# Optimization experiments

Hardware: AMD Instinct MI355X
Metric: run time of the kernel (lower is better)

Reference implementation:

```python
import jax, jax.numpy as jnp
import numpy as np

B, T, L = 512, 512, 128  # batch, seq_len, tag-vocab size (incl. START=126, STOP=127)


def setup_inputs() -> dict:
    key = jax.random.key(0)
    k1, k2, k3 = jax.random.split(key, 3)
    # scale emissions so exp(gold path score) stays finite in fp32
    feats = jax.random.normal(k1, (B, T, L), dtype=jnp.float32) * 0.05
    # xavier_normal on [L, L] -> std = sqrt(2/(L+L)) = 1/sqrt(L)
    transfer = jax.random.normal(k2, (L, L), dtype=jnp.float32) * (1.0 / np.sqrt(L))
    target = jax.random.randint(k3, (B, T), 0, L - 2, dtype=jnp.int32)
    return {"feats": feats, "transfer": transfer, "target": target,
            "start": L - 2, "stop": L - 1}


def _crf_loss(feats, transfer, target, start, stop):
    # feats: [B, T, L] emissions; transfer: [L, L]; target: [B, T] gold tags
    Bb, Tt, Ll = feats.shape

    # ---- forward algorithm (log-sum-exp DP over tags) ----
    # scores[1] = feats[1] + transfer[start, :]
    prev0 = feats[:, 1] + transfer[start][None, :]  # [B, L]

    def step(prev, f_t):
        # original: scores[t, y] = LSE_x( scores[t-1, x] + feats[t, x] + transfer[x, y] )
        v = prev + f_t                                        # [B, L] over prev-tag x
        new = jax.nn.logsumexp(v[:, :, None] + transfer[None, :, :], axis=1)  # [B, L]
        return new, None

    step = jax.checkpoint(step)  # keep scan residuals to just the carries
    feats_rest = jnp.swapaxes(feats[:, 2:], 0, 1)  # [T-2, B, L]
    prev, _ = jax.lax.scan(step, prev0, feats_rest)
    sentence_score = jax.nn.logsumexp(prev + transfer[:, stop][None, :], axis=1)  # [B]

    # ---- gold path score ----
    emit0 = feats[:, 0, start]  # hh[0, start]
    emit = jnp.take_along_axis(feats[:, 1:], target[:, 1:, None], axis=2)[..., 0].sum(axis=1)
    pre = jnp.concatenate(
        [jnp.full((Bb, 1), start, dtype=target.dtype), target[:, 1:Tt - 1]], axis=1)  # [B, T-1]
    # original reads transfer[pre, tgt].data[0] -> detached constant
    trans = jax.lax.stop_gradient(transfer[pre, target[:, 1:]]).sum(axis=1)
    gold_score = jnp.exp(emit0 + emit + trans)  # original returns torch.exp(score)

    return sentence_score - gold_score  # per-sentence loss, shape [B]


def reference(feats, transfer, target, start, stop):
    return _crf_loss(feats, transfer, target, start, stop)
```

## Files before the change

### kernel.cpp

```cpp
#include <hip/hip_runtime.h>
#include <hip/hip_bf16.h>

#define T_DIM 512
#define L_DIM 128

typedef _Float16 h2 __attribute__((ext_vector_type(2)));

#if defined(__has_builtin)
#if __has_builtin(__builtin_amdgcn_fdot2)
#define HAS_FDOT2 1
#endif
#endif

__device__ __forceinline__ float fdot2_acc(h2 a, h2 b, float c) {
#ifdef HAS_FDOT2
    return __builtin_amdgcn_fdot2(a, b, c, false);
#else
    return c + (float)a.x * (float)b.x + (float)a.y * (float)b.y;
#endif
}

__device__ __forceinline__ h2 pack_f16(float a, float b) {
    return __builtin_bit_cast(h2, __builtin_amdgcn_cvt_pkrtz(a, b));
}

__device__ __forceinline__ h2 uint_as_h2(unsigned int v) {
    return __builtin_bit_cast(h2, v);
}

__global__ __launch_bounds__(64, 1) void crf_fwd_kernel(
    const float* __restrict__ feats,
    const float* __restrict__ transfer,
    const int* __restrict__ target,
    const int* __restrict__ startp,
    const int* __restrict__ stopp,
    float* __restrict__ out)
{
    __shared__ unsigned int LdsU[2][64] __attribute__((aligned(16)));

    const int lane = threadIdx.x;
    const int p    = lane;
    const int j0   = p << 1;
    const int b    = blockIdx.x;
    const int start = startp[0];
    const int stop  = stopp[0];
    const float* fbase = feats + (size_t)b * T_DIM * L_DIM;
    const float2* f2 = reinterpret_cast<const float2*>(fbase);
    const float LOG128 = 4.852030263919617f;

    h2 E0[64], E1[64];
#pragma unroll
    for (int q = 0; q < 64; ++q) {
        const float2* r0 = reinterpret_cast<const float2*>(transfer + (2 * q) * L_DIM + j0);
        const float2* r1 = reinterpret_cast<const float2*>(transfer + (2 * q + 1) * L_DIM + j0);
        float2 e0 = *r0;
        float2 e1 = *r1;
        E0[q] = pack_f16(__expf(e0.x) * 0.0078125f, __expf(e1.x) * 0.0078125f);
        E1[q] = pack_f16(__expf(e0.y) * 0.0078125f, __expf(e1.y) * 0.0078125f);
    }
    const float trS0 = transfer[j0 * L_DIM + stop];
    const float trS1 = transfer[(j0 | 1) * L_DIM + stop];

    {
        float2 f1v = f2[1 * 64 + p];
        float2 f2v = f2[2 * 64 + p];
        const float2* ts = reinterpret_cast<const float2*>(transfer + start * L_DIM + j0);
        float2 tsv = *ts;
        LdsU[0][p] = __builtin_bit_cast(unsigned int,
                        pack_f16(__expf(f1v.x + f2v.x + tsv.x),
                                 __expf(f1v.y + f2v.y + tsv.y)));
    }
    float2 fa = f2[3 * 64 + p];
    float2 fb = f2[4 * 64 + p];
    float S = 0.f;

    int cur = 0;
    float accF0 = 0.f, accF1 = 0.f;

    for (int t = 2; t <= T_DIM - 1; ++t) {
        int tp = t + 3; if (tp > T_DIM - 1) tp = T_DIM - 1;
        float2 fnew = f2[tp * 64 + p];
        float fe0 = __expf(fa.x);
        float fe1 = __expf(fa.y);

        asm volatile("s_waitcnt lgkmcnt(0)" ::: "memory");
        const uint4* P4 = reinterpret_cast<const uint4*>(&LdsU[cur][0]);

        float a0 = 0.f, a1 = 0.f, a2 = 0.f, a3 = 0.f;
        float c0 = 0.f, c1 = 0.f, c2 = 0.f, c3 = 0.f;
        bool renorm = ((t & 15) == 0);

#pragma unroll
        for (int g = 0; g < 4; ++g) {
            uint4 q0 = P4[4 * g + 0];
            uint4 q1 = P4[4 * g + 1];
            uint4 q2 = P4[4 * g + 2];
            uint4 q3 = P4[4 * g + 3];
            if (g == 0 && renorm) {
                float u0 = (float)uint_as_h2(q0.x).x;
                float rr = __builtin_amdgcn_rcpf(u0);
                S += __logf(u0);
                fe0 *= rr; fe1 *= rr;
            }
#pragma unroll
            for (int r = 0; r < 4; ++r) {
                uint4 qq = (r == 0) ? q0 : (r == 1) ? q1 : (r == 2) ? q2 : q3;
                int e = 16 * g + 4 * r;
                h2 u0p = uint_as_h2(qq.x);
                h2 u1p = uint_as_h2(qq.y);
                h2 u2p = uint_as_h2(qq.z);
                h2 u3p = uint_as_h2(qq.w);
                a0 = fdot2_acc(u0p, E0[e + 0], a0);
                a1 = fdot2_acc(u1p, E0[e + 1], a1);
                a2 = fdot2_acc(u2p, E0[e + 2], a2);
                a3 = fdot2_acc(u3p, E0[e + 3], a3);
                c0 = fdot2_acc(u0p, E1[e + 0], c0);
                c1 = fdot2_acc(u1p, E1[e + 1], c1);
                c2 = fdot2_acc(u2p, E1[e + 2], c2);
                c3 = fdot2_acc(u3p, E1[e + 3], c3);
            }
        }
        float acc0 = (a0 + a1) + (a2 + a3);
        float acc1 = (c0 + c1) + (c2 + c3);

        if (t < T_DIM - 1) {
            float un0 = acc0 * fe0;
            float un1 = acc1 * fe1;
            fa = fb; fb = fnew;
            LdsU[cur ^ 1][p] = __builtin_bit_cast(unsigned int, pack_f16(un0, un1));
            cur ^= 1;
        } else {
            accF0 = acc0; accF1 = acc1;
        }
    }

    S += 510.0f * LOG128;

    float x0 = __logf(accF0) + S + trS0;
    float x1 = __logf(accF1) + S + trS1;
    float mx = fmaxf(x0, x1);
#pragma unroll
    for (int d = 1; d < 64; d <<= 1) mx = fmaxf(mx, __shfl_xor(mx, d));
    float ex = __expf(x0 - mx) + __expf(x1 - mx);
#pragma unroll
    for (int d = 1; d < 64; d <<= 1) ex += __shfl_xor(ex, d);
    float sentence = mx + __logf(ex);

    float es = 0.f, ts = 0.f;
#pragma unroll
    for (int k = 0; k < 8; ++k) {
        int t = 1 + lane + (k << 6);
        if (t < T_DIM) {
            int tg = target[b * T_DIM + t];
            es += fbase[t * L_DIM + tg];
            int pr = (t == 1) ? start : target[b * T_DIM + t - 1];
            ts += transfer[pr * L_DIM + tg];
        }
    }
#pragma unroll
    for (int d = 1; d < 64; d <<= 1) {
        es += __shfl_xor(es, d);
        ts += __shfl_xor(ts, d);
    }

    if (lane == 0) {
        float emit0 = fbase[start];
        out[b] = sentence - __expf(emit0 + es + ts);
    }
}

extern "C" void kernel_launch(void* const* d_in, const int* in_sizes, int n_in,
                              void* d_out, int out_size, void* d_ws, size_t ws_size,
                              hipStream_t stream) {
    const float* feats    = (const float*)d_in[0];
    const float* transfer = (const float*)d_in[1];
    const int*   target   = (const int*)d_in[2];
    const int*   startp   = (const int*)d_in[3];
    const int*   stopp    = (const int*)d_in[4];
    float* outp = (float*)d_out;
    int B = in_sizes[0] / (T_DIM * L_DIM);
    hipLaunchKernelGGL(crf_fwd_kernel, dim3(B), dim3(64), 0, stream,
                       feats, transfer, target, startp, stopp, outp);
}
```

Measured before the change: 397.1 us.

## Split CRF forward DP across two wavefronts with barrier-synchronised LDS exchange

The forward log-sum-exp recursion now runs with 128 threads per batch element instead of 64. Each thread owns one output tag, which halves the per-thread fdot2 work and the transfer-matrix register footprint. This adds an s_barrier every timestep so both wavefronts see the new state vector. The feature prefetch distance is also deepened, and the final reductions combine the two wavefronts through LDS. The goal is to shorten the serial per-step critical path, at the cost of a workgroup barrier per step and 16-bit LDS stores.

```diff
diff --git a/kernel.cpp b/kernel.cpp
--- a/kernel.cpp
+++ b/kernel.cpp
@@ -28,7 +28,11 @@
     return __builtin_bit_cast(h2, v);
 }
 
-__global__ __launch_bounds__(64, 1) void crf_fwd_kernel(
+__device__ __forceinline__ void lds_barrier() {
+    asm volatile("s_waitcnt lgkmcnt(0)\n\ts_barrier" ::: "memory");
+}
+
+__global__ __launch_bounds__(128, 1) void crf_fwd_kernel(
     const float* __restrict__ feats,
     const float* __restrict__ transfer,
     const int* __restrict__ target,
@@ -37,57 +41,51 @@
     float* __restrict__ out)
 {
     __shared__ unsigned int LdsU[2][64] __attribute__((aligned(16)));
+    __shared__ float LdsRed[8];
 
-    const int lane = threadIdx.x;
-    const int p    = lane;
-    const int j0   = p << 1;
+    const int tid  = threadIdx.x;
+    const int lane = tid & 63;
+    const int wv   = tid >> 6;
+    const int j    = (lane << 1) | wv;
     const int b    = blockIdx.x;
     const int start = startp[0];
     const int stop  = stopp[0];
     const float* fbase = feats + (size_t)b * T_DIM * L_DIM;
-    const float2* f2 = reinterpret_cast<const float2*>(fbase);
     const float LOG128 = 4.852030263919617f;
 
-    h2 E0[64], E1[64];
+    h2 E[64];
 #pragma unroll
     for (int q = 0; q < 64; ++q) {
-        const float2* r0 = reinterpret_cast<const float2*>(transfer + (2 * q) * L_DIM + j0);
-        const float2* r1 = reinterpret_cast<const float2*>(transfer + (2 * q + 1) * L_DIM + j0);
-        float2 e0 = *r0;
-        float2 e1 = *r1;
-        E0[q] = pack_f16(__expf(e0.x) * 0.0078125f, __expf(e1.x) * 0.0078125f);
-        E1[q] = pack_f16(__expf(e0.y) * 0.0078125f, __expf(e1.y) * 0.0078125f);
+        float e0 = __expf(transfer[(2 * q)     * L_DIM + j]) * 0.0078125f;
+        float e1 = __expf(transfer[(2 * q + 1) * L_DIM + j]) * 0.0078125f;
+        E[q] = pack_f16(e0, e1);
     }
-    const float trS0 = transfer[j0 * L_DIM + stop];
-    const float trS1 = transfer[(j0 | 1) * L_DIM + stop];
+    const float trS = transfer[j * L_DIM + stop];
 
     {
-        float2 f1v = f2[1 * 64 + p];
-        float2 f2v = f2[2 * 64 + p];
-        const float2* ts = reinterpret_cast<const float2*>(transfer + start * L_DIM + j0);
-        float2 tsv = *ts;
-        LdsU[0][p] = __builtin_bit_cast(unsigned int,
-                        pack_f16(__expf(f1v.x + f2v.x + tsv.x),
-                                 __expf(f1v.y + f2v.y + tsv.y)));
+        float v2 = fbase[1 * L_DIM + j] + fbase[2 * L_DIM + j]
+                 + transfer[start * L_DIM + j];
+        reinterpret_cast<unsigned short*>(&LdsU[0][0])[j] =
+            __builtin_bit_cast(unsigned short, (_Float16)__expf(v2));
     }
-    float2 fa = f2[3 * 64 + p];
-    float2 fb = f2[4 * 64 + p];
+    float fa  = fbase[3 * L_DIM + j];
+    float fb_ = fbase[4 * L_DIM + j];
+    float fc  = fbase[5 * L_DIM + j];
+    float fd  = fbase[6 * L_DIM + j];
     float S = 0.f;
+    lds_barrier();
 
     int cur = 0;
-    float accF0 = 0.f, accF1 = 0.f;
+    float accF = 0.f;
 
+#pragma unroll 4
     for (int t = 2; t <= T_DIM - 1; ++t) {
-        int tp = t + 3; if (tp > T_DIM - 1) tp = T_DIM - 1;
-        float2 fnew = f2[tp * 64 + p];
-        float fe0 = __expf(fa.x);
-        float fe1 = __expf(fa.y);
+        int tp = t + 5; if (tp > T_DIM - 1) tp = T_DIM - 1;
+        float fnew = fbase[tp * L_DIM + j];
+        float fe = __expf(fa);
 
-        asm volatile("s_waitcnt lgkmcnt(0)" ::: "memory");
         const uint4* P4 = reinterpret_cast<const uint4*>(&LdsU[cur][0]);
-
         float a0 = 0.f, a1 = 0.f, a2 = 0.f, a3 = 0.f;
-        float c0 = 0.f, c1 = 0.f, c2 = 0.f, c3 = 0.f;
         bool renorm = ((t & 15) == 0);
 
 #pragma unroll
@@ -100,56 +98,54 @@
                 float u0 = (float)uint_as_h2(q0.x).x;
                 float rr = __builtin_amdgcn_rcpf(u0);
                 S += __logf(u0);
-                fe0 *= rr; fe1 *= rr;
+                fe *= rr;
             }
-#pragma unroll
-            for (int r = 0; r < 4; ++r) {
-                uint4 qq = (r == 0) ? q0 : (r == 1) ? q1 : (r == 2) ? q2 : q3;
-                int e = 16 * g + 4 * r;
-                h2 u0p = uint_as_h2(qq.x);
-                h2 u1p = uint_as_h2(qq.y);
-                h2 u2p = uint_as_h2(qq.z);
-                h2 u3p = uint_as_h2(qq.w);
-                a0 = fdot2_acc(u0p, E0[e + 0], a0);
-                a1 = fdot2_acc(u1p, E0[e + 1], a1);
-                a2 = fdot2_acc(u2p, E0[e + 2], a2);
-                a3 = fdot2_acc(u3p, E0[e + 3], a3);
-                c0 = fdot2_acc(u0p, E1[e + 0], c0);
-                c1 = fdot2_acc(u1p, E1[e + 1], c1);
-                c2 = fdot2_acc(u2p, E1[e + 2], c2);
-                c3 = fdot2_acc(u3p, E1[e + 3], c3);
-            }
+            int e = g << 4;
+            a0 = fdot2_acc(uint_as_h2(q0.x), E[e + 0],  a0);
+            a1 = fdot2_acc(uint_as_h2(q0.y), E[e + 1],  a1);
+            a2 = fdot2_acc(uint_as_h2(q0.z), E[e + 2],  a2);
+            a3 = fdot2_acc(uint_as_h2(q0.w), E[e + 3],  a3);
+            a0 = fdot2_acc(uint_as_h2(q1.x), E[e + 4],  a0);
+            a1 = fdot2_acc(uint_as_h2(q1.y), E[e + 5],  a1);
+            a2 = fdot2_acc(uint_as_h2(q1.z), E[e + 6],  a2);
+            a3 = fdot2_acc(uint_as_h2(q1.w), E[e + 7],  a3);
+            a0 = fdot2_acc(uint_as_h2(q2.x), E[e + 8],  a0);
+            a1 = fdot2_acc(uint_as_h2(q2.y), E[e + 9],  a1);
+            a2 = fdot2_acc(uint_as_h2(q2.z), E[e + 10], a2);
+            a3 = fdot2_acc(uint_as_h2(q2.w), E[e + 11], a3);
+            a0 = fdot2_acc(uint_as_h2(q3.x), E[e + 12], a0);
+            a1 = fdot2_acc(uint_as_h2(q3.y), E[e + 13], a1);
+            a2 = fdot2_acc(uint_as_h2(q3.z), E[e + 14], a2);
+            a3 = fdot2_acc(uint_as_h2(q3.w), E[e + 15], a3);
         }
-        float acc0 = (a0 + a1) + (a2 + a3);
-        float acc1 = (c0 + c1) + (c2 + c3);
+        float acc = (a0 + a1) + (a2 + a3);
 
         if (t < T_DIM - 1) {
-            float un0 = acc0 * fe0;
-            float un1 = acc1 * fe1;
-            fa = fb; fb = fnew;
-            LdsU[cur ^ 1][p] = __builtin_bit_cast(unsigned int, pack_f16(un0, un1));
+            float un = acc * fe;
+            fa = fb_; fb_ = fc; fc = fd; fd = fnew;
+            reinterpret_cast<unsigned short*>(&LdsU[cur ^ 1][0])[j] =
+                __builtin_bit_cast(unsigned short, (_Float16)un);
+            lds_barrier();
             cur ^= 1;
         } else {
-            accF0 = acc0; accF1 = acc1;
+            accF = acc;
         }
     }
 
     S += 510.0f * LOG128;
 
-    float x0 = __logf(accF0) + S + trS0;
-    float x1 = __logf(accF1) + S + trS1;
-    float mx = fmaxf(x0, x1);
+    float x  = __logf(accF) + S + trS;
+    float mx = x;
 #pragma unroll
     for (int d = 1; d < 64; d <<= 1) mx = fmaxf(mx, __shfl_xor(mx, d));
-    float ex = __expf(x0 - mx) + __expf(x1 - mx);
+    float ex = __expf(x - mx);
 #pragma unroll
     for (int d = 1; d < 64; d <<= 1) ex += __shfl_xor(ex, d);
-    float sentence = mx + __logf(ex);
 
     float es = 0.f, ts = 0.f;
 #pragma unroll
-    for (int k = 0; k < 8; ++k) {
-        int t = 1 + lane + (k << 6);
+    for (int k = 0; k < 4; ++k) {
+        int t = 1 + tid + (k << 7);
         if (t < T_DIM) {
             int tg = target[b * T_DIM + t];
             es += fbase[t * L_DIM + tg];
@@ -164,8 +160,19 @@
     }
 
     if (lane == 0) {
+        LdsRed[wv] = mx; LdsRed[2 + wv] = ex;
+        LdsRed[4 + wv] = es; LdsRed[6 + wv] = ts;
+    }
+    __syncthreads();
+
+    if (tid == 0) {
+        float M  = fmaxf(LdsRed[0], LdsRed[1]);
+        float Sm = LdsRed[2] * __expf(LdsRed[0] - M)
+                 + LdsRed[3] * __expf(LdsRed[1] - M);
+        float sentence = M + __logf(Sm);
         float emit0 = fbase[start];
-        out[b] = sentence - __expf(emit0 + es + ts);
+        out[b] = sentence - __expf(emit0 + LdsRed[4] + LdsRed[5]
+                                         + LdsRed[6] + LdsRed[7]);
     }
 }
 
@@ -179,6 +186,6 @@
     const int*   stopp    = (const int*)d_in[4];
     float* outp = (float*)d_out;
     int B = in_sizes[0] / (T_DIM * L_DIM);
-    hipLaunchKernelGGL(crf_fwd_kernel, dim3(B), dim3(64), 0, stream,
+    hipLaunchKernelGGL(crf_fwd_kernel, dim3(B), dim3(128), 0, stream,
                        feats, transfer, target, startp, stopp, outp);
 }
```

Measured after the change: 456.9 us. 1.15x slower.
